# Performance work log

Measured on AMD Instinct MI355X. Metric: run time of the kernel, lower is better.

The kernel has to match this reference:

```python
import jax, jax.numpy as jnp
import numpy as np

HEADS = 16
DIM_HEAD = 64
SCALE = DIM_HEAD ** -0.5


def setup_inputs() -> dict:
    key = jax.random.key(0)
    k1, k2, k3 = jax.random.split(key, 3)
    B, N, D = 8, 1024, 1024
    x = jax.random.normal(k1, (B, N, D), dtype=jnp.float32)
    # 0/1 keep-mask over the N-1 non-prepended positions
    mask = jax.random.randint(k2, (B, N - 1), 0, 2, dtype=jnp.int32)
    # Linear(dim, 3*inner_dim, bias=False); stored as [dim, 3*inner] so y = x @ W
    w_qkv = jax.random.normal(k3, (D, 3 * HEADS * DIM_HEAD), dtype=jnp.float32) * (D ** -0.5)
    return {"x": x, "mask": mask, "w_qkv": w_qkv}


def reference(x, mask, w_qkv):
    b, n, _ = x.shape
    h, d = HEADS, DIM_HEAD
    qkv = x @ w_qkv                                    # [b, n, 3*h*d]
    q, k, v = jnp.split(qkv, 3, axis=-1)
    to_heads = lambda t: t.reshape(b, n, h, d).transpose(0, 2, 1, 3)  # b h n d
    q, k, v = to_heads(q), to_heads(k), to_heads(v)
    dots = jnp.einsum('bhid,bhjd->bhij', q, k) * SCALE  # [b, h, n, n]
    # F.pad(mask.flatten(1), (1,0), value=1.0) -> prepend a kept position
    m = jnp.pad(mask.reshape(b, -1).astype(jnp.float32), ((0, 0), (1, 0)),
                constant_values=1.0)                    # [b, n]
    dots = dots - 10000.0 * (1.0 - m)[:, None, None, :]
    attn = jax.nn.softmax(dots, axis=-1)
    out = jnp.einsum('bhij,bhjd->bhid', attn, v)        # [b, h, n, d]
    return out.transpose(0, 2, 1, 3).reshape(b, n, h * d)
```

## Files before the change

kernel.cpp:

```cpp
#include <hip/hip_runtime.h>
#include <hip/hip_bf16.h>
#include <stdint.h>

#define HEADS 16
#define DH    64
#define SEQ   1024
#define DIM   1024

typedef __attribute__((ext_vector_type(8))) short bf16x8;
typedef __attribute__((ext_vector_type(4))) float f32x4;
typedef __attribute__((ext_vector_type(16))) float f32x16;
typedef __attribute__((ext_vector_type(4))) unsigned int u32x4;

#define QSCALE_L2 0.18033688011112042f
#define THR_L2 11.541560327111707f
#define PEN_L2 (-14427.0f)

static __device__ __forceinline__ unsigned short f2bf(float f) {
  unsigned u = __builtin_bit_cast(unsigned, f);
  u += 0x7fff + ((u >> 16) & 1);
  return (unsigned short)(u >> 16);
}

static __device__ __forceinline__ float fexp2(float x) {
#if __has_builtin(__builtin_amdgcn_exp2f)
  return __builtin_amdgcn_exp2f(x);
#else
  return exp2f(x);
#endif
}

static __device__ __forceinline__ void gload_lds16(const void* g, void* l) {
  __builtin_amdgcn_global_load_lds(
      (const __attribute__((address_space(1))) unsigned int*)g,
      (__attribute__((address_space(3))) unsigned int*)l,
      16, 0, 0);
}

__global__ __launch_bounds__(256) void prep(
    const float* __restrict__ x, unsigned short* __restrict__ xb,
    const float* __restrict__ w, unsigned short* __restrict__ wT,
    const int* __restrict__ mask, int* __restrict__ inv,
    int* __restrict__ nkeep) {
  __shared__ unsigned short t[64][68];
  __shared__ int sc[256];
  const int bidx = blockIdx.x;
  const int tid = threadIdx.x;

  if (bidx < 8192) {
    const int i = (bidx * 256 + tid) * 4;
    const float4 v = *reinterpret_cast<const float4*>(x + i);
    short4 o;
    o.x = (short)f2bf(v.x);
    o.y = (short)f2bf(v.y);
    o.z = (short)f2bf(v.z);
    o.w = (short)f2bf(v.w);
    *reinterpret_cast<short4*>(xb + i) = o;
  } else if (bidx < 8960) {
    const int lin = bidx - 8192;
    const int bk = lin & 15;
    const int bn = lin >> 4;
    const int r = tid >> 4;
    const int c = (tid & 15) * 4;
#pragma unroll
    for (int rr = 0; rr < 64; rr += 16) {
      const float4 v = *reinterpret_cast<const float4*>(
          w + (size_t)(bk * 64 + r + rr) * 3072 + bn * 64 + c);
      t[r + rr][c + 0] = f2bf(v.x);
      t[r + rr][c + 1] = f2bf(v.y);
      t[r + rr][c + 2] = f2bf(v.z);
      t[r + rr][c + 3] = f2bf(v.w);
    }
    __syncthreads();
#pragma unroll
    for (int rr = 0; rr < 64; rr += 16) {
      short4 o;
      o.x = (short)t[c + 0][r + rr];
      o.y = (short)t[c + 1][r + rr];
      o.z = (short)t[c + 2][r + rr];
      o.w = (short)t[c + 3][r + rr];
      *reinterpret_cast<short4*>(
          wT + (size_t)(bn * 64 + r + rr) * 1024 + bk * 64 + c) = o;
    }
  } else {
    const int b = bidx - 8960;
    int kept[4];
    int c = 0;
#pragma unroll
    for (int k = 0; k < 4; ++k) {
      const int j = tid * 4 + k;
      const int kp = (j == 0) ? 1 : (mask[b * (SEQ - 1) + j - 1] != 0);
      kept[k] = kp;
      c += kp;
    }
    sc[tid] = c;
    __syncthreads();
    for (int off = 1; off < 256; off <<= 1) {
      const int v = (tid >= off) ? sc[tid - off] : 0;
      __syncthreads();
      sc[tid] += v;
      __syncthreads();
    }
    int pos = sc[tid] - c;
    const int total = sc[255];
#pragma unroll
    for (int k = 0; k < 4; ++k) {
      const int j = tid * 4 + k;
      inv[b * SEQ + j] = kept[k] ? pos : -1;
      pos += kept[k];
    }
    if (tid == 0) nkeep[b] = total;
  }
}

__global__ __launch_bounds__(256, 2) void qkv_gemm(
    const unsigned short* __restrict__ x, const unsigned short* __restrict__ wT,
    const int* __restrict__ inv,
    unsigned short* __restrict__ Qh, unsigned short* __restrict__ Kc,
    unsigned short* __restrict__ Vc) {
  __shared__ alignas(16) unsigned char La[256 * 128];
  __shared__ alignas(16) unsigned char Lb[128 * 128];
  const int tid = threadIdx.x;
  const int lane = tid & 63;
  const int wave = tid >> 6;
  const int m0 = blockIdx.x * 256;
  const int n0 = blockIdx.y * 128;
  const int wm = (wave >> 1) * 128;
  const int wn = (wave & 1) * 64;
  const int l15 = lane & 15;
  const int lg = lane >> 4;
  const int lg4 = lg * 4;

  f32x4 acc[8][4] = {};

  auto STAGE = [&](int kt) {
#pragma unroll
    for (int r = 0; r < 8; ++r) {
      const int o = r * 4096 + tid * 16;
      const int row = o >> 7;
      const int sch = ((o >> 4) & 7) ^ (row & 7);
      gload_lds16(x + (size_t)(m0 + row) * DIM + kt + sch * 8, La + o);
    }
#pragma unroll
    for (int r = 0; r < 4; ++r) {
      const int o = r * 4096 + tid * 16;
      const int row = o >> 7;
      const int sch = ((o >> 4) & 7) ^ (row & 7);
      gload_lds16(wT + (size_t)(n0 + row) * DIM + kt + sch * 8, Lb + o);
    }
  };

  for (int t = 0; t < 16; ++t) {
    const int kt = t * 64;
    __syncthreads();
    STAGE(kt);
    __syncthreads();
#pragma unroll
    for (int kk = 0; kk < 2; ++kk) {
      bf16x8 af[8], bfr[4];
#pragma unroll
      for (int i = 0; i < 8; ++i) {
        const int ra = wm + i * 16 + l15;
        af[i] = *reinterpret_cast<const bf16x8*>(
            La + ra * 128 + (((kk * 4 + lg) ^ (ra & 7)) << 4));
      }
#pragma unroll
      for (int j = 0; j < 4; ++j) {
        const int rb = wn + j * 16 + l15;
        bfr[j] = *reinterpret_cast<const bf16x8*>(
            Lb + rb * 128 + (((kk * 4 + lg) ^ (rb & 7)) << 4));
      }
#pragma unroll
      for (int i = 0; i < 8; ++i)
#pragma unroll
        for (int j = 0; j < 4; ++j)
          acc[i][j] = __builtin_amdgcn_mfma_f32_16x16x32_bf16(
              af[i], bfr[j], acc[i][j], 0, 0, 0);
    }
  }

  __syncthreads();
  unsigned short* Sw = reinterpret_cast<unsigned short*>(La + wave * 2304);
  const int sec = n0 >> 10;
  const float sc = (sec == 0) ? QSCALE_L2 : 1.0f;
  const int h = ((n0 + wn) >> 6) & 15;
#pragma unroll
  for (int i = 0; i < 8; ++i) {
#pragma unroll
    for (int j = 0; j < 4; ++j)
#pragma unroll
      for (int r = 0; r < 4; ++r)
        Sw[(lg4 + r) * 72 + j * 16 + l15] = f2bf(acc[i][j][r] * sc);
#pragma unroll
    for (int pass = 0; pass < 2; ++pass) {
      const int row = pass * 8 + (lane >> 3);
      const int chunk = lane & 7;
      const bf16x8 vv = *reinterpret_cast<const bf16x8*>(&Sw[row * 72 + chunk * 8]);
      const int grow = m0 + wm + i * 16 + row;
      const int b = grow >> 10;
      const int n = grow & 1023;
      const size_t bh = (size_t)b * HEADS + h;
      if (sec == 0) {
        *reinterpret_cast<bf16x8*>(&Qh[(bh * SEQ + n) * DH + chunk * 8]) = vv;
      } else {
        const int iv = inv[b * SEQ + n];
        if (iv >= 0) {
          if (sec == 1)
            *reinterpret_cast<bf16x8*>(&Kc[(bh * SEQ + iv) * DH + chunk * 8]) = vv;
          else
            *reinterpret_cast<bf16x8*>(&Vc[(bh * SEQ + iv) * DH + chunk * 8]) = vv;
        }
      }
    }
  }
}

__global__ __launch_bounds__(256) void transpose_v(
    const unsigned short* __restrict__ Vc, unsigned short* __restrict__ Vtc) {
  __shared__ unsigned short t[64][72];
  const int tid = threadIdx.x;
  const int i0 = blockIdx.x * 64;
  const int bhi = blockIdx.y;
  const unsigned short* src = Vc + (size_t)bhi * SEQ * DH;
  unsigned short* dst = Vtc + (size_t)bhi * DH * SEQ;
  const int r = tid >> 3;
  const int c = (tid & 7) * 8;
#pragma unroll
  for (int rr = 0; rr < 64; rr += 32) {
    const bf16x8 v = *reinterpret_cast<const bf16x8*>(
        src + (size_t)(i0 + r + rr) * DH + c);
    *reinterpret_cast<bf16x8*>(&t[r + rr][c]) = v;
  }
  __syncthreads();
#pragma unroll
  for (int dd = 0; dd < 64; dd += 32) {
    const int d = r + dd;
    bf16x8 o;
#pragma unroll
    for (int e = 0; e < 8; ++e) o[e] = (short)t[c + e][d];
    *reinterpret_cast<bf16x8*>(dst + (size_t)d * SEQ + i0 + c) = o;
  }
}

__global__ __launch_bounds__(256) void attn_fwd5(
    const unsigned short* __restrict__ Qh, const unsigned short* __restrict__ Kc,
    const unsigned short* __restrict__ Vtc,
    const int* __restrict__ nkeep, float* __restrict__ out) {
  __shared__ alignas(16) unsigned char Kl[2][8192];
  __shared__ alignas(16) unsigned char Vl[2][8192];
  __shared__ float corrw[4][32];
  const int tid = threadIdx.x;
  const int lane = tid & 63;
  const int wave = tid >> 6;
  const int l31 = lane & 31;
  const int hi = lane >> 5;
  const int h8 = hi * 8;
  const bool islo = lane < 32;

  const int bid = ((blockIdx.x & 7) << 7) | (blockIdx.x >> 3);
  const int b = bid >> 7;
  const int hh = (bid >> 3) & 15;
  const int qc = bid & 7;
  const size_t bh = (size_t)b * HEADS + hh;
  const int q0 = qc * 128 + wave * 32;

  const int nk = nkeep[b];
  const int ntile = (nk + 63) >> 6;

  const unsigned short* Q = Qh + bh * SEQ * DH;
  const unsigned short* K = Kc + bh * SEQ * DH;
  const unsigned short* V = Vtc + bh * DH * SEQ;

  auto STAGE = [&](int buf, int kt) {
#pragma unroll
    for (int p = 0; p < 2; ++p) {
      const int off = p * 4096 + tid * 16;
      const int row = off >> 7;
      const int chunk = (off >> 4) & 7;
      const int sch = chunk ^ (row & 7);
      gload_lds16(K + (size_t)(kt + row) * DH + sch * 8, &Kl[buf][off]);
      gload_lds16(V + (size_t)row * SEQ + kt + sch * 8, &Vl[buf][off]);
    }
  };

  STAGE(0, 0);

  bf16x8 qf[4];
#pragma unroll
  for (int ds = 0; ds < 4; ++ds)
    qf[ds] = *reinterpret_cast<const bf16x8*>(
        Q + (size_t)(q0 + l31) * DH + ds * 16 + h8);

  u32x4 onesu = {0u, 0u, 0u, 0u};
  onesu.x = islo ? 0x3F80u : 0u;
  const bf16x8 onesf = __builtin_bit_cast(bf16x8, onesu);

  f32x16 Od0 = (f32x16)0.f, Od1 = (f32x16)0.f;
  float m_ = 0.f, l_ = 0.f;

  __syncthreads();

  int cur = 0;
  for (int ti = 0; ti < ntile; ++ti) {
    const int kt = ti * 64;
    if (ti + 1 < ntile) STAGE(cur ^ 1, kt + 64);

    f32x16 st0 = (f32x16)0.f, st1 = (f32x16)0.f;
    __builtin_amdgcn_s_setprio(1);
#pragma unroll
    for (int ds = 0; ds < 4; ++ds) {
      const int c0 = (ds * 2 + hi) ^ (l31 & 7);
      const bf16x8 kf0 = *reinterpret_cast<const bf16x8*>(
          &Kl[cur][l31 * 128 + c0 * 16]);
      st0 = __builtin_amdgcn_mfma_f32_32x32x16_bf16(kf0, qf[ds], st0, 0, 0, 0);
      const bf16x8 kf1 = *reinterpret_cast<const bf16x8*>(
          &Kl[cur][(32 + l31) * 128 + c0 * 16]);
      st1 = __builtin_amdgcn_mfma_f32_32x32x16_bf16(kf1, qf[ds], st1, 0, 0, 0);
    }
    __builtin_amdgcn_s_setprio(0);

    if (ti == ntile - 1) {
      const unsigned short pv = f2bf(PEN_L2);
      const unsigned short pu0 = (kt + l31 < nk) ? (unsigned short)0 : pv;
      const unsigned short pu1 = (kt + 32 + l31 < nk) ? (unsigned short)0 : pv;
      u32x4 p0 = {0u, 0u, 0u, 0u}, p1 = {0u, 0u, 0u, 0u};
      p0.x = islo ? (unsigned)pu0 : 0u;
      p1.x = islo ? (unsigned)pu1 : 0u;
      st0 = __builtin_amdgcn_mfma_f32_32x32x16_bf16(
          __builtin_bit_cast(bf16x8, p0), onesf, st0, 0, 0, 0);
      st1 = __builtin_amdgcn_mfma_f32_32x32x16_bf16(
          __builtin_bit_cast(bf16x8, p1), onesf, st1, 0, 0, 0);
    }
    float a[8];
#pragma unroll
    for (int i = 0; i < 8; ++i)
      a[i] = fmaxf(fmaxf(st0[i], st0[i + 8]), fmaxf(st1[i], st1[i + 8]));
#pragma unroll
    for (int k = 4; k >= 1; k >>= 1)
#pragma unroll
      for (int i = 0; i < k; ++i) a[i] = fmaxf(a[i], a[i + k]);
    const float mx = fmaxf(a[0], __shfl_xor(a[0], 32));
    if (!__all(mx <= m_ + THR_L2)) {
      const float mn = fmaxf(m_, mx);
      const float corr = fexp2(m_ - mn);
      m_ = mn;
      l_ *= corr;
      if (islo) corrw[wave][l31] = corr;
      f32x4 cv[4];
#pragma unroll
      for (int j = 0; j < 4; ++j)
        cv[j] = *reinterpret_cast<const f32x4*>(&corrw[wave][j * 8 + (h8 >> 1)]);
#pragma unroll
      for (int r = 0; r < 16; ++r) {
        Od0[r] *= cv[r >> 2][r & 3];
        Od1[r] *= cv[r >> 2][r & 3];
      }
    }
#pragma unroll
    for (int i = 0; i < 16; ++i) {
      st0[i] = fexp2(st0[i] - m_);
      st1[i] = fexp2(st1[i] - m_);
    }
    float s8[8];
#pragma unroll
    for (int i = 0; i < 8; ++i)
      s8[i] = (st0[i] + st0[i + 8]) + (st1[i] + st1[i + 8]);
#pragma unroll
    for (int k = 4; k >= 1; k >>= 1)
#pragma unroll
      for (int i = 0; i < k; ++i) s8[i] += s8[i + k];
    l_ += s8[0] + __shfl_xor(s8[0], 32);
    bf16x8 pf[4];
#pragma unroll
    for (int t = 0; t < 2; ++t) {
#pragma unroll
      for (int bq = 0; bq < 2; ++bq) {
        const int o = 8 * bq;
        float e0 = t ? st1[o + 0] : st0[o + 0], e1 = t ? st1[o + 1] : st0[o + 1];
        float e2 = t ? st1[o + 2] : st0[o + 2], e3 = t ? st1[o + 3] : st0[o + 3];
        float e4 = t ? st1[o + 4] : st0[o + 4], e5 = t ? st1[o + 5] : st0[o + 5];
        float e6 = t ? st1[o + 6] : st0[o + 6], e7 = t ? st1[o + 7] : st0[o + 7];
        unsigned A0, A1, B0, B1;
        asm("v_cvt_pk_bf16_f32 %0, %1, %2" : "=v"(A0) : "v"(e0), "v"(e1));
        asm("v_cvt_pk_bf16_f32 %0, %1, %2" : "=v"(A1) : "v"(e2), "v"(e3));
        asm("v_cvt_pk_bf16_f32 %0, %1, %2" : "=v"(B0) : "v"(e4), "v"(e5));
        asm("v_cvt_pk_bf16_f32 %0, %1, %2" : "=v"(B1) : "v"(e6), "v"(e7));
        asm("v_permlane32_swap_b32 %0, %1\n\ts_nop 1" : "+v"(A0), "+v"(B0));
        asm("v_permlane32_swap_b32 %0, %1\n\ts_nop 1" : "+v"(A1), "+v"(B1));
        u32x4 pk4;
        pk4.x = A0; pk4.y = A1; pk4.z = B0; pk4.w = B1;
        pf[t * 2 + bq] = __builtin_bit_cast(bf16x8, pk4);
      }
    }
    __builtin_amdgcn_s_setprio(1);
#pragma unroll
    for (int kvs = 0; kvs < 4; ++kvs) {
      const int c0 = (kvs * 2 + hi) ^ (l31 & 7);
      const bf16x8 v0 = *reinterpret_cast<const bf16x8*>(
          &Vl[cur][l31 * 128 + c0 * 16]);
      Od0 = __builtin_amdgcn_mfma_f32_32x32x16_bf16(pf[kvs], v0, Od0, 0, 0, 0);
      const bf16x8 v1 = *reinterpret_cast<const bf16x8*>(
          &Vl[cur][(32 + l31) * 128 + c0 * 16]);
      Od1 = __builtin_amdgcn_mfma_f32_32x32x16_bf16(pf[kvs], v1, Od1, 0, 0, 0);
    }
    __builtin_amdgcn_s_setprio(0);

    __syncthreads();
    cur ^= 1;
  }

  if (islo) corrw[wave][l31] = 1.0f / l_;
  f32x4 lv[4];
#pragma unroll
  for (int j = 0; j < 4; ++j)
    lv[j] = *reinterpret_cast<const f32x4*>(&corrw[wave][j * 8 + (h8 >> 1)]);
#pragma unroll
  for (int r = 0; r < 16; ++r) {
    const int q = q0 + (r & 3) + 8 * (r >> 2) + (hi << 2);
    out[((size_t)b * SEQ + q) * (HEADS * DH) + hh * DH + 0 * 32 + l31] =
        Od0[r] * lv[r >> 2][r & 3];
    out[((size_t)b * SEQ + q) * (HEADS * DH) + hh * DH + 1 * 32 + l31] =
        Od1[r] * lv[r >> 2][r & 3];
  }
}

extern "C" void kernel_launch(void* const* d_in, const int* in_sizes, int n_in,
                              void* d_out, int out_size, void* d_ws, size_t ws_size,
                              hipStream_t stream) {
  const float* x = (const float*)d_in[0];
  const int* mask = (const int*)d_in[1];
  const float* w = (const float*)d_in[2];
  float* outp = (float*)d_out;

  char* ws = (char*)d_ws;
  unsigned short* xb   = (unsigned short*)(ws);
  unsigned short* wT   = (unsigned short*)(ws + 16777216);
  unsigned short* Qh   = (unsigned short*)(ws + 23068672);
  unsigned short* Kc   = (unsigned short*)(ws + 39845888);
  unsigned short* Vc   = (unsigned short*)(ws + 56623104);
  int*            inv  = (int*)(ws + 73400320);
  int*            nkp  = (int*)(ws + 73433088);
  unsigned short* Vtc  = xb;

  prep<<<dim3(8968), 256, 0, stream>>>(x, xb, w, wT, mask, inv, nkp);
  qkv_gemm<<<dim3(32, 24), 256, 0, stream>>>(xb, wT, inv, Qh, Kc, Vc);
  transpose_v<<<dim3(16, 128), 256, 0, stream>>>(Vc, Vtc);
  attn_fwd5<<<dim3(1024), 256, 0, stream>>>(Qh, Kc, Vtc, nkp, outp);
}
```

Measured before the change: 125.7 us.

## Compute K/V projections only for kept rows via gathered compact GEMM

The prep kernel now writes a compacted list of kept positions instead of an inverse map. The QKV GEMM becomes a 1D grid: Q tiles are computed over all rows, while K/V tiles gather only the kept input rows per batch and skip whole tiles past the kept count. This removes roughly half of the K/V GEMM work for a mask that is about half ones. In exchange it adds indirect row loads, and the grid is imbalanced because early-exiting blocks leave the remaining work uneven.

```diff
diff --git a/kernel.cpp b/kernel.cpp
--- a/kernel.cpp
+++ b/kernel.cpp
@@ -40,7 +40,7 @@
 __global__ __launch_bounds__(256) void prep(
     const float* __restrict__ x, unsigned short* __restrict__ xb,
     const float* __restrict__ w, unsigned short* __restrict__ wT,
-    const int* __restrict__ mask, int* __restrict__ inv,
+    const int* __restrict__ mask, int* __restrict__ kl,
     int* __restrict__ nkeep) {
   __shared__ unsigned short t[64][68];
   __shared__ int sc[256];
@@ -106,7 +106,7 @@
 #pragma unroll
     for (int k = 0; k < 4; ++k) {
       const int j = tid * 4 + k;
-      inv[b * SEQ + j] = kept[k] ? pos : -1;
+      if (kept[k]) kl[b * SEQ + pos] = j;
       pos += kept[k];
     }
     if (tid == 0) nkeep[b] = total;
@@ -115,7 +115,7 @@
 
 __global__ __launch_bounds__(256, 2) void qkv_gemm(
     const unsigned short* __restrict__ x, const unsigned short* __restrict__ wT,
-    const int* __restrict__ inv,
+    const int* __restrict__ kl, const int* __restrict__ nkeep,
     unsigned short* __restrict__ Qh, unsigned short* __restrict__ Kc,
     unsigned short* __restrict__ Vc) {
   __shared__ alignas(16) unsigned char La[256 * 128];
@@ -123,13 +123,41 @@
   const int tid = threadIdx.x;
   const int lane = tid & 63;
   const int wave = tid >> 6;
-  const int m0 = blockIdx.x * 256;
-  const int n0 = blockIdx.y * 128;
+  const int bq = blockIdx.x;
+
+  int m0, n0, nkb;
+  int srow[8];
+  const int rbase = tid >> 3;
+  if (bq < 256) {
+    m0 = (bq >> 3) * 256;
+    n0 = (bq & 7) * 128;
+    nkb = 1 << 30;
+#pragma unroll
+    for (int r = 0; r < 8; ++r) srow[r] = m0 + r * 32 + rbase;
+  } else {
+    const int idx = bq - 256;
+    const int b = idx >> 6;
+    const int mt = (idx >> 4) & 3;
+    const int nt = idx & 15;
+    nkb = nkeep[b];
+    const int m0c = mt * 256;
+    if (m0c >= nkb) return;
+    m0 = b * 1024 + m0c;
+    n0 = 1024 + nt * 128;
+#pragma unroll
+    for (int r = 0; r < 8; ++r) {
+      int i = m0c + r * 32 + rbase;
+      i = (i < nkb) ? i : (nkb - 1);
+      srow[r] = b * 1024 + kl[b * SEQ + i];
+    }
+  }
+
   const int wm = (wave >> 1) * 128;
   const int wn = (wave & 1) * 64;
   const int l15 = lane & 15;
   const int lg = lane >> 4;
   const int lg4 = lg * 4;
+  const int scha = (tid & 7) ^ ((tid >> 3) & 7);
 
   f32x4 acc[8][4] = {};
 
@@ -137,16 +165,13 @@
 #pragma unroll
     for (int r = 0; r < 8; ++r) {
       const int o = r * 4096 + tid * 16;
-      const int row = o >> 7;
-      const int sch = ((o >> 4) & 7) ^ (row & 7);
-      gload_lds16(x + (size_t)(m0 + row) * DIM + kt + sch * 8, La + o);
+      gload_lds16(x + (size_t)srow[r] * DIM + kt + scha * 8, La + o);
     }
 #pragma unroll
     for (int r = 0; r < 4; ++r) {
       const int o = r * 4096 + tid * 16;
-      const int row = o >> 7;
-      const int sch = ((o >> 4) & 7) ^ (row & 7);
-      gload_lds16(wT + (size_t)(n0 + row) * DIM + kt + sch * 8, Lb + o);
+      gload_lds16(wT + (size_t)(n0 + r * 32 + rbase) * DIM + kt + scha * 8,
+                  Lb + o);
     }
   };
 
@@ -202,14 +227,11 @@
       const size_t bh = (size_t)b * HEADS + h;
       if (sec == 0) {
         *reinterpret_cast<bf16x8*>(&Qh[(bh * SEQ + n) * DH + chunk * 8]) = vv;
-      } else {
-        const int iv = inv[b * SEQ + n];
-        if (iv >= 0) {
-          if (sec == 1)
-            *reinterpret_cast<bf16x8*>(&Kc[(bh * SEQ + iv) * DH + chunk * 8]) = vv;
-          else
-            *reinterpret_cast<bf16x8*>(&Vc[(bh * SEQ + iv) * DH + chunk * 8]) = vv;
-        }
+      } else if (n < nkb) {
+        if (sec == 1)
+          *reinterpret_cast<bf16x8*>(&Kc[(bh * SEQ + n) * DH + chunk * 8]) = vv;
+        else
+          *reinterpret_cast<bf16x8*>(&Vc[(bh * SEQ + n) * DH + chunk * 8]) = vv;
       }
     }
   }
@@ -438,12 +460,12 @@
   unsigned short* Qh   = (unsigned short*)(ws + 23068672);
   unsigned short* Kc   = (unsigned short*)(ws + 39845888);
   unsigned short* Vc   = (unsigned short*)(ws + 56623104);
-  int*            inv  = (int*)(ws + 73400320);
+  int*            kl   = (int*)(ws + 73400320);
   int*            nkp  = (int*)(ws + 73433088);
   unsigned short* Vtc  = xb;
 
-  prep<<<dim3(8968), 256, 0, stream>>>(x, xb, w, wT, mask, inv, nkp);
-  qkv_gemm<<<dim3(32, 24), 256, 0, stream>>>(xb, wT, inv, Qh, Kc, Vc);
+  prep<<<dim3(8968), 256, 0, stream>>>(x, xb, w, wT, mask, kl, nkp);
+  qkv_gemm<<<dim3(768), 256, 0, stream>>>(xb, wT, kl, nkp, Qh, Kc, Vc);
   transpose_v<<<dim3(16, 128), 256, 0, stream>>>(Vc, Vtc);
   attn_fwd5<<<dim3(1024), 256, 0, stream>>>(Qh, Kc, Vtc, nkp, outp);
 }
```

Measured after the change: 125.2 us. Within noise of the previous version (-0.4%).
